# Performance work log

Hardware: AMD Instinct MI355X
Metric: run time of the kernel (lower is better)

## Reference

```python
import jax, jax.numpy as jnp
import numpy as np

N_NODES = 100000


def gcn_conv(x, src, dst, norm, W, b):
    # PyG GCNConv: linear transform first, then normalized scatter-add aggregation, then bias.
    xw = x @ W                                   # [N, out]
    msgs = xw[src] * norm[:, None]               # [E+N, out] gathered, degree-normalized messages
    out = jax.ops.segment_sum(msgs, dst, num_segments=N_NODES)
    return out + b


def _build_graph(edge_index):
    # add self-loops (PyG gcn_norm default)
    loop = jnp.arange(N_NODES, dtype=edge_index.dtype)
    src = jnp.concatenate([edge_index[0], loop])
    dst = jnp.concatenate([edge_index[1], loop])
    deg = jax.ops.segment_sum(jnp.ones_like(dst, dtype=jnp.float32), dst, num_segments=N_NODES)
    dis = jnp.where(deg > 0, jax.lax.rsqrt(jnp.maximum(deg, 1.0)), 0.0)
    norm = dis[src] * dis[dst]                   # D^-1/2 (A+I) D^-1/2 edge weights
    return src, dst, norm


def setup_inputs() -> dict:
    key = jax.random.key(0)
    ks = jax.random.split(key, 6)
    F_IN, H, C, E = 128, 128, 8, 1600000
    x = jax.random.normal(ks[0], (N_NODES, F_IN), dtype=jnp.float32)
    edge_index = jax.random.randint(ks[1], (2, E), 0, N_NODES, dtype=jnp.int64)
    # glorot-style init for conv weights
    W1 = jax.random.normal(ks[2], (F_IN, H), dtype=jnp.float32) * (1.0 / np.sqrt(F_IN))
    b1 = jnp.zeros((H,), dtype=jnp.float32)
    W2 = jax.random.normal(ks[3], (H, C), dtype=jnp.float32) * (1.0 / np.sqrt(H))
    b2 = jnp.zeros((C,), dtype=jnp.float32)
    return {"x": x, "edge_index": edge_index, "W1": W1, "b1": b1, "W2": W2, "b2": b2}


def reference(x, edge_index, W1, b1, W2, b2):
    src, dst, norm = _build_graph(edge_index)
    h = gcn_conv(x, src, dst, norm, W1, b1)
    h = jax.nn.relu(h)
    # dropout is identity in eval mode
    out = gcn_conv(h, src, dst, norm, W2, b2)
    return jax.nn.log_softmax(out, axis=1)
```

## Files before the change

### kernel.cpp

```cpp
#include <hip/hip_runtime.h>

#define N_NODES 100000
#define NBKT 782
#define EPB 8192
#define SL_STRIDE 800000

typedef unsigned int uint;

__device__ __forceinline__ uint pack_bf16_2(float a, float b) {
    uint ua = __float_as_uint(a), ub = __float_as_uint(b);
    ua += 0x7fff + ((ua >> 16) & 1);
    ub += 0x7fff + ((ub >> 16) & 1);
    return (ua >> 16) | (ub & 0xffff0000u);
}
__device__ __forceinline__ float bf_lo(uint u) { return __uint_as_float(u << 16); }
__device__ __forceinline__ float bf_hi(uint u) { return __uint_as_float(u & 0xffff0000u); }

__device__ __forceinline__ int edge_at(const int* __restrict__ ei, int idx, int is64) {
    return is64 ? ei[2 * idx] : ei[idx];
}

__global__ void k_zero(int* __restrict__ bkt_cnt, int* __restrict__ flag,
                       const int* __restrict__ ei, float* __restrict__ y2) {
    int i = blockIdx.x * 256 + threadIdx.x;
    if (i < NBKT) bkt_cnt[i] = 0;
    if (i < N_NODES * 8) y2[i] = 0.0f;
    if (blockIdx.x == 0) {
        if (threadIdx.x == 0) flag[0] = 0;
        __syncthreads();
        int any = 0;
        for (int j = threadIdx.x; j < 4096; j += 256) any |= ei[2 * j + 1];
        if (any) atomicOr(flag, 1);
    }
}

__global__ __launch_bounds__(256) void kA1(const int* __restrict__ ei, int E,
                                           const int* __restrict__ flag,
                                           int* __restrict__ bkt_cnt) {
    __shared__ int h[NBKT];
    int t = threadIdx.x;
    for (int i = t; i < NBKT; i += 256) h[i] = 0;
    __syncthreads();
    int is64 = (flag[0] == 0);
    int base = blockIdx.x * EPB;
    int end = min(base + EPB, E);
    for (int e = base + t; e < end; e += 256) {
        int d = edge_at(ei, E + e, is64);
        atomicAdd(&h[d >> 7], 1);
    }
    __syncthreads();
    for (int i = t; i < NBKT; i += 256)
        if (h[i]) atomicAdd(&bkt_cnt[i], h[i]);
}

__global__ __launch_bounds__(1024) void kA2(const int* __restrict__ bkt_cnt,
                                            int* __restrict__ bkt_off,
                                            int* __restrict__ bkt_cursor) {
    __shared__ int s[1024];
    int t = threadIdx.x;
    int v = (t < NBKT) ? bkt_cnt[t] : 0;
    s[t] = v;
    __syncthreads();
    for (int d = 1; d < 1024; d <<= 1) {
        int y = (t >= d) ? s[t - d] : 0;
        __syncthreads();
        s[t] += y;
        __syncthreads();
    }
    if (t < NBKT) {
        int o = s[t] - v;
        bkt_off[t] = o;
        bkt_cursor[t] = o;
    }
}

__global__ __launch_bounds__(256) void kA3(const int* __restrict__ ei, int E,
                                           const int* __restrict__ flag,
                                           int* __restrict__ bkt_cursor,
                                           uint* __restrict__ bkt_data) {
    __shared__ int h[NBKT];
    __shared__ int base[NBKT];
    int t = threadIdx.x;
    for (int i = t; i < NBKT; i += 256) h[i] = 0;
    __syncthreads();
    int is64 = (flag[0] == 0);
    int lo = blockIdx.x * EPB;
    int end = min(lo + EPB, E);
    for (int e = lo + t; e < end; e += 256) {
        int d = edge_at(ei, E + e, is64);
        atomicAdd(&h[d >> 7], 1);
    }
    __syncthreads();
    for (int i = t; i < NBKT; i += 256) {
        int c = h[i];
        base[i] = c ? atomicAdd(&bkt_cursor[i], c) : 0;
    }
    __syncthreads();
    for (int i = t; i < NBKT; i += 256) h[i] = 0;
    __syncthreads();
    for (int e = lo + t; e < end; e += 256) {
        int d = edge_at(ei, E + e, is64);
        int s = edge_at(ei, e, is64);
        int b = d >> 7;
        int r = atomicAdd(&h[b], 1);
        bkt_data[base[b] + r] = ((uint)s << 7) | (uint)(d & 127);
    }
}

__global__ __launch_bounds__(256) void kB(const uint* __restrict__ bkt_data,
                                          const int* __restrict__ bkt_off,
                                          const int* __restrict__ bkt_cnt,
                                          int* __restrict__ srcs,
                                          int* __restrict__ count,
                                          int* __restrict__ offs,
                                          float* __restrict__ dis) {
    __shared__ int lc[128];
    __shared__ int sc[128];
    __shared__ int lcur[128];
    int t = threadIdx.x;
    int b = blockIdx.x;
    if (t < 128) { lc[t] = 0; lcur[t] = 0; }
    __syncthreads();
    int start = bkt_off[b];
    int n = bkt_cnt[b];
    for (int i = t; i < n; i += 256)
        atomicAdd(&lc[bkt_data[start + i] & 127], 1);
    __syncthreads();
    if (t < 128) sc[t] = lc[t];
    __syncthreads();
    for (int d = 1; d < 128; d <<= 1) {
        int y = 0;
        if (t < 128 && t >= d) y = sc[t - d];
        __syncthreads();
        if (t < 128) sc[t] += y;
        __syncthreads();
    }
    if (t < 128) {
        int node = b * 128 + t;
        if (node < N_NODES) {
            int c = lc[t];
            count[node] = c;
            offs[node] = start + sc[t] - c;
            dis[node] = rsqrtf((float)c + 1.0f);
        }
    }
    __syncthreads();
    for (int i = t; i < n; i += 256) {
        uint rec = bkt_data[start + i];
        int dl = rec & 127;
        int r = atomicAdd(&lcur[dl], 1);
        srcs[start + (sc[dl] - lc[dl]) + r] = rec >> 7;
    }
}

__global__ __launch_bounds__(256) void k_gemm1(const float* __restrict__ x,
                                               const float* __restrict__ W,
                                               const float* __restrict__ dis,
                                               uint* __restrict__ y1s) {
    __shared__ float Wl[64 * 128];
    __shared__ float Xl[32 * 128];
    int t = threadIdx.x;
    int row0 = blockIdx.x * 32;

    const float4* X4 = (const float4*)(x + (size_t)row0 * 128);
    float4* Xl4 = (float4*)Xl;
#pragma unroll
    for (int i = 0; i < 4; ++i) Xl4[t + 256 * i] = X4[t + 256 * i];

    int cg = t & 31;
    int rg = t >> 5;
    float acc[4][4] = {};
    float4* Wl4 = (float4*)Wl;
    const float4* W4 = (const float4*)W;

    for (int kh = 0; kh < 2; ++kh) {
        __syncthreads();
#pragma unroll
        for (int i = 0; i < 8; ++i) Wl4[t + 256 * i] = W4[kh * 2048 + t + 256 * i];
        __syncthreads();
        for (int k = 0; k < 64; ++k) {
            float4 w = Wl4[k * 32 + cg];
#pragma unroll
            for (int r = 0; r < 4; ++r) {
                float xv = Xl[(4 * rg + r) * 128 + kh * 64 + k];
                acc[r][0] = fmaf(xv, w.x, acc[r][0]);
                acc[r][1] = fmaf(xv, w.y, acc[r][1]);
                acc[r][2] = fmaf(xv, w.z, acc[r][2]);
                acc[r][3] = fmaf(xv, w.w, acc[r][3]);
            }
        }
    }
    int slice = cg >> 2, sp = cg & 3;
#pragma unroll
    for (int r = 0; r < 4; ++r) {
        int row = row0 + 4 * rg + r;
        float dd = dis[row];
        uint2 o;
        o.x = pack_bf16_2(acc[r][0] * dd, acc[r][1] * dd);
        o.y = pack_bf16_2(acc[r][2] * dd, acc[r][3] * dd);
        ((uint2*)y1s)[(size_t)slice * (SL_STRIDE / 2) + row * 4 + sp] = o;
    }
}

__global__ __launch_bounds__(256) void k_agg1s(const uint* __restrict__ y1s,
                                               const int* __restrict__ srcs,
                                               const int* __restrict__ offs,
                                               const int* __restrict__ count,
                                               const float* __restrict__ dis,
                                               const float* __restrict__ b1,
                                               const float* __restrict__ W2,
                                               float* __restrict__ y2) {
    int t = threadIdx.x;
    int slice = blockIdx.x & 7;
    int nb = blockIdx.x >> 3;
    int g = t >> 3;
    int j = t & 7;
    int d = nb * 32 + g;

    float w0[8], w1[8];
    const float* wr0 = W2 + (size_t)(slice * 16 + 2 * j) * 8;
#pragma unroll
    for (int c = 0; c < 8; ++c) { w0[c] = wr0[c]; w1[c] = wr0[8 + c]; }

    const uint4* ybase = (const uint4*)(y1s + (size_t)slice * SL_STRIDE);
    float acc[16];
#pragma unroll
    for (int c = 0; c < 16; ++c) acc[c] = 0.0f;

    int st = offs[d], n = count[d];
    for (int i = j; i <= n; i += 8) {
        int sk = d;
        if (i < n) sk = srcs[st + i];
        uint4 a  = ybase[(size_t)sk * 2];
        uint4 bq = ybase[(size_t)sk * 2 + 1];
        acc[0]  += bf_lo(a.x);  acc[1]  += bf_hi(a.x);
        acc[2]  += bf_lo(a.y);  acc[3]  += bf_hi(a.y);
        acc[4]  += bf_lo(a.z);  acc[5]  += bf_hi(a.z);
        acc[6]  += bf_lo(a.w);  acc[7]  += bf_hi(a.w);
        acc[8]  += bf_lo(bq.x); acc[9]  += bf_hi(bq.x);
        acc[10] += bf_lo(bq.y); acc[11] += bf_hi(bq.y);
        acc[12] += bf_lo(bq.z); acc[13] += bf_hi(bq.z);
        acc[14] += bf_lo(bq.w); acc[15] += bf_hi(bq.w);
    }

    int hi4 = (j >> 2) & 1, hi2 = (j >> 1) & 1, hi1 = j & 1;
    float v8[8];
#pragma unroll
    for (int c = 0; c < 8; ++c) {
        float keep = hi4 ? acc[c + 8] : acc[c];
        float send = hi4 ? acc[c] : acc[c + 8];
        v8[c] = keep + __shfl_xor(send, 4, 8);
    }
    float v4[4];
#pragma unroll
    for (int c = 0; c < 4; ++c) {
        float keep = hi2 ? v8[c + 4] : v8[c];
        float send = hi2 ? v8[c] : v8[c + 4];
        v4[c] = keep + __shfl_xor(send, 2, 8);
    }
    float v2[2];
#pragma unroll
    for (int c = 0; c < 2; ++c) {
        float keep = hi1 ? v4[c + 2] : v4[c];
        float send = hi1 ? v4[c] : v4[c + 2];
        v2[c] = keep + __shfl_xor(send, 1, 8);
    }

    float dd = dis[d];
    float2 b = ((const float2*)b1)[slice * 8 + j];
    float h0 = fmaxf(fmaf(v2[0], dd, b.x), 0.0f);
    float h1 = fmaxf(fmaf(v2[1], dd, b.y), 0.0f);

    float p[8];
#pragma unroll
    for (int c = 0; c < 8; ++c) p[c] = h0 * w0[c] + h1 * w1[c];
    float q4[4];
#pragma unroll
    for (int c = 0; c < 4; ++c) {
        float keep = hi4 ? p[c + 4] : p[c];
        float send = hi4 ? p[c] : p[c + 4];
        q4[c] = keep + __shfl_xor(send, 4, 8);
    }
    float q2[2];
#pragma unroll
    for (int c = 0; c < 2; ++c) {
        float keep = hi2 ? q4[c + 2] : q4[c];
        float send = hi2 ? q4[c] : q4[c + 2];
        q2[c] = keep + __shfl_xor(send, 2, 8);
    }
    float keep = hi1 ? q2[1] : q2[0];
    float send = hi1 ? q2[0] : q2[1];
    float q = keep + __shfl_xor(send, 1, 8);

    atomicAdd(&y2[(size_t)d * 8 + j], q * dd);
}

__global__ __launch_bounds__(256) void k_agg2(const float* __restrict__ y2,
                                              const int* __restrict__ srcs,
                                              const int* __restrict__ offs,
                                              const int* __restrict__ count,
                                              const float* __restrict__ dis,
                                              const float* __restrict__ b2,
                                              float* __restrict__ out) {
    int g = (blockIdx.x * 256 + threadIdx.x) >> 3;
    int c = threadIdx.x & 7;
    if (g >= N_NODES) return;
    float acc = y2[(size_t)g * 8 + c];
    float acc2 = 0.0f;
    int st = offs[g], n = count[g];
    int i = 0;
    for (; i + 2 <= n; i += 2) {
        int s0 = srcs[st + i], s1 = srcs[st + i + 1];
        acc  += y2[(size_t)s0 * 8 + c];
        acc2 += y2[(size_t)s1 * 8 + c];
    }
    if (i < n) acc += y2[(size_t)srcs[st + i] * 8 + c];
    acc += acc2;

    float o = fmaf(acc, dis[g], b2[c]);
    float m = o;
#pragma unroll
    for (int k = 1; k < 8; k <<= 1) m = fmaxf(m, __shfl_xor(m, k, 64));
    float e = expf(o - m);
    float ssum = e;
#pragma unroll
    for (int k = 1; k < 8; k <<= 1) ssum += __shfl_xor(ssum, k, 64);
    out[(size_t)g * 8 + c] = (o - m) - logf(ssum);
}

extern "C" void kernel_launch(void* const* d_in, const int* in_sizes, int n_in,
                              void* d_out, int out_size, void* d_ws, size_t ws_size,
                              hipStream_t stream) {
    const float* x  = (const float*)d_in[0];
    const int*   ei = (const int*)d_in[1];
    const float* W1 = (const float*)d_in[2];
    const float* b1 = (const float*)d_in[3];
    const float* W2 = (const float*)d_in[4];
    const float* b2 = (const float*)d_in[5];
    float* out = (float*)d_out;
    const int E = in_sizes[1] / 2;

    char* ws = (char*)d_ws;
    int*   flag       = (int*)ws;
    int*   bkt_cnt    = (int*)(ws + 256);
    int*   bkt_off    = bkt_cnt + 784;
    int*   bkt_cursor = bkt_off + 784;
    int*   count      = bkt_cursor + 784;
    int*   offs       = count + N_NODES;
    float* dis        = (float*)(offs + N_NODES);
    uint*  bkt_data   = (uint*)(dis + N_NODES);
    int*   srcs       = (int*)(bkt_data + E);
    uint*  y1s        = (uint*)(srcs + E);
    float* y2         = (float*)(y1s + (size_t)8 * SL_STRIDE);

    const int PB = (E + EPB - 1) / EPB;

    k_zero <<<3125, 256, 0, stream>>>(bkt_cnt, flag, ei, y2);
    kA1    <<<PB, 256, 0, stream>>>(ei, E, flag, bkt_cnt);
    kA2    <<<1, 1024, 0, stream>>>(bkt_cnt, bkt_off, bkt_cursor);
    kA3    <<<PB, 256, 0, stream>>>(ei, E, flag, bkt_cursor, bkt_data);
    kB     <<<NBKT, 256, 0, stream>>>(bkt_data, bkt_off, bkt_cnt, srcs, count, offs, dis);

    k_gemm1<<<N_NODES / 32, 256, 0, stream>>>(x, W1, dis, y1s);
    k_agg1s<<<8 * 3125, 256, 0, stream>>>(y1s, srcs, offs, count, dis, b1, W2, y2);
    k_agg2 <<<(N_NODES + 31) / 32, 256, 0, stream>>>(y2, srcs, offs, count, dis, b2, out);
}
```

Baseline: 226.1 us.

## Use bf16 MFMA for first GEMM, unroll aggregation gather, vectorize zeroing

```diff
diff --git a/kernel.cpp b/kernel.cpp
--- a/kernel.cpp
+++ b/kernel.cpp
@@ -6,6 +6,10 @@
 #define SL_STRIDE 800000
 
 typedef unsigned int uint;
+typedef __attribute__((ext_vector_type(8))) short bf16x8;
+typedef __attribute__((ext_vector_type(4))) float f32x4;
+
+union FragU { uint4 u; bf16x8 b; };
 
 __device__ __forceinline__ uint pack_bf16_2(float a, float b) {
     uint ua = __float_as_uint(a), ub = __float_as_uint(b);
@@ -21,10 +25,10 @@
 }
 
 __global__ void k_zero(int* __restrict__ bkt_cnt, int* __restrict__ flag,
-                       const int* __restrict__ ei, float* __restrict__ y2) {
+                       const int* __restrict__ ei, float4* __restrict__ y2q) {
     int i = blockIdx.x * 256 + threadIdx.x;
     if (i < NBKT) bkt_cnt[i] = 0;
-    if (i < N_NODES * 8) y2[i] = 0.0f;
+    if (i < N_NODES * 2) y2q[i] = make_float4(0.f, 0.f, 0.f, 0.f);
     if (blockIdx.x == 0) {
         if (threadIdx.x == 0) flag[0] = 0;
         __syncthreads();
@@ -157,48 +161,80 @@
                                                const float* __restrict__ W,
                                                const float* __restrict__ dis,
                                                uint* __restrict__ y1s) {
-    __shared__ float Wl[64 * 128];
-    __shared__ float Xl[32 * 128];
-    int t = threadIdx.x;
-    int row0 = blockIdx.x * 32;
-
-    const float4* X4 = (const float4*)(x + (size_t)row0 * 128);
-    float4* Xl4 = (float4*)Xl;
-#pragma unroll
-    for (int i = 0; i < 4; ++i) Xl4[t + 256 * i] = X4[t + 256 * i];
-
-    int cg = t & 31;
-    int rg = t >> 5;
-    float acc[4][4] = {};
-    float4* Wl4 = (float4*)Wl;
+    __shared__ uint4 WtA[2048];
+    char* wt = (char*)WtA;
+    int t = threadIdx.x;
+
     const float4* W4 = (const float4*)W;
-
-    for (int kh = 0; kh < 2; ++kh) {
-        __syncthreads();
-#pragma unroll
-        for (int i = 0; i < 8; ++i) Wl4[t + 256 * i] = W4[kh * 2048 + t + 256 * i];
-        __syncthreads();
-        for (int k = 0; k < 64; ++k) {
-            float4 w = Wl4[k * 32 + cg];
-#pragma unroll
-            for (int r = 0; r < 4; ++r) {
-                float xv = Xl[(4 * rg + r) * 128 + kh * 64 + k];
-                acc[r][0] = fmaf(xv, w.x, acc[r][0]);
-                acc[r][1] = fmaf(xv, w.y, acc[r][1]);
-                acc[r][2] = fmaf(xv, w.z, acc[r][2]);
-                acc[r][3] = fmaf(xv, w.w, acc[r][3]);
+#pragma unroll
+    for (int ii = 0; ii < 4; ++ii) {
+        int tile = t + 256 * ii;
+        int nq = tile >> 5, kq = tile & 31;
+        float4 r0 = W4[(4 * kq + 0) * 32 + nq];
+        float4 r1 = W4[(4 * kq + 1) * 32 + nq];
+        float4 r2 = W4[(4 * kq + 2) * 32 + nq];
+        float4 r3 = W4[(4 * kq + 3) * 32 + nq];
+        const float* p0 = (const float*)&r0;
+        const float* p1 = (const float*)&r1;
+        const float* p2 = (const float*)&r2;
+        const float* p3 = (const float*)&r3;
+#pragma unroll
+        for (int cc = 0; cc < 4; ++cc) {
+            int n = 4 * nq + cc;
+            uint2 v;
+            v.x = pack_bf16_2(p0[cc], p1[cc]);
+            v.y = pack_bf16_2(p2[cc], p3[cc]);
+            *(uint2*)(wt + n * 256 + (((kq >> 1) ^ (n & 7)) << 4) + ((kq & 1) << 3)) = v;
+        }
+    }
+    __syncthreads();
+
+    int w = t >> 6, lane = t & 63;
+    int m = lane & 15, kg = lane >> 4;
+    int row0 = blockIdx.x * 64 + 16 * w;
+
+    int arow = row0 + m;
+    bool av = arow < N_NODES;
+    const float4* xr = (const float4*)(x + (size_t)arow * 128);
+    float4 z4 = make_float4(0.f, 0.f, 0.f, 0.f);
+    FragU af[4];
+#pragma unroll
+    for (int kf = 0; kf < 4; ++kf) {
+        float4 g0 = av ? xr[8 * kf + 2 * kg]     : z4;
+        float4 g1 = av ? xr[8 * kf + 2 * kg + 1] : z4;
+        const float* a0 = (const float*)&g0;
+        const float* a1 = (const float*)&g1;
+        af[kf].u.x = pack_bf16_2(a0[0], a0[1]);
+        af[kf].u.y = pack_bf16_2(a0[2], a0[3]);
+        af[kf].u.z = pack_bf16_2(a1[0], a1[1]);
+        af[kf].u.w = pack_bf16_2(a1[2], a1[3]);
+    }
+
+    int crow = row0 + 4 * kg;
+    float dd[4];
+#pragma unroll
+    for (int rr = 0; rr < 4; ++rr)
+        dd[rr] = (crow + rr < N_NODES) ? dis[crow + rr] : 0.0f;
+
+#pragma unroll
+    for (int ct = 0; ct < 8; ++ct) {
+        f32x4 acc = {0.f, 0.f, 0.f, 0.f};
+#pragma unroll
+        for (int kf = 0; kf < 4; ++kf) {
+            int n = 16 * ct + m;
+            bf16x8 bw = *(const bf16x8*)(wt + n * 256 + ((((kf << 2) | kg) ^ (n & 7)) << 4));
+            acc = __builtin_amdgcn_mfma_f32_16x16x32_bf16(af[kf].b, bw, acc, 0, 0, 0);
+        }
+#pragma unroll
+        for (int rr = 0; rr < 4; ++rr) {
+            float v = acc[rr] * dd[rr];
+            float p = __shfl_xor(v, 1, 64);
+            if (!(lane & 1)) {
+                int grow = crow + rr;
+                if (grow < N_NODES)
+                    y1s[(size_t)ct * SL_STRIDE + grow * 8 + (m >> 1)] = pack_bf16_2(v, p);
             }
         }
-    }
-    int slice = cg >> 2, sp = cg & 3;
-#pragma unroll
-    for (int r = 0; r < 4; ++r) {
-        int row = row0 + 4 * rg + r;
-        float dd = dis[row];
-        uint2 o;
-        o.x = pack_bf16_2(acc[r][0] * dd, acc[r][1] * dd);
-        o.y = pack_bf16_2(acc[r][2] * dd, acc[r][3] * dd);
-        ((uint2*)y1s)[(size_t)slice * (SL_STRIDE / 2) + row * 4 + sp] = o;
     }
 }
 
@@ -228,10 +264,26 @@
     for (int c = 0; c < 16; ++c) acc[c] = 0.0f;
 
     int st = offs[d], n = count[d];
-    for (int i = j; i <= n; i += 8) {
-        int sk = d;
-        if (i < n) sk = srcs[st + i];
-        uint4 a  = ybase[(size_t)sk * 2];
+    int i = j;
+    for (; i + 8 <= n; i += 16) {
+        int s0 = srcs[st + i];
+        int s1 = (i + 8 < n) ? srcs[st + i + 8] : d;
+        uint4 a0 = ybase[(size_t)s0 * 2];
+        uint4 b0 = ybase[(size_t)s0 * 2 + 1];
+        uint4 a1 = ybase[(size_t)s1 * 2];
+        uint4 b1q = ybase[(size_t)s1 * 2 + 1];
+        acc[0]  += bf_lo(a0.x) + bf_lo(a1.x);  acc[1]  += bf_hi(a0.x) + bf_hi(a1.x);
+        acc[2]  += bf_lo(a0.y) + bf_lo(a1.y);  acc[3]  += bf_hi(a0.y) + bf_hi(a1.y);
+        acc[4]  += bf_lo(a0.z) + bf_lo(a1.z);  acc[5]  += bf_hi(a0.z) + bf_hi(a1.z);
+        acc[6]  += bf_lo(a0.w) + bf_lo(a1.w);  acc[7]  += bf_hi(a0.w) + bf_hi(a1.w);
+        acc[8]  += bf_lo(b0.x) + bf_lo(b1q.x); acc[9]  += bf_hi(b0.x) + bf_hi(b1q.x);
+        acc[10] += bf_lo(b0.y) + bf_lo(b1q.y); acc[11] += bf_hi(b0.y) + bf_hi(b1q.y);
+        acc[12] += bf_lo(b0.z) + bf_lo(b1q.z); acc[13] += bf_hi(b0.z) + bf_hi(b1q.z);
+        acc[14] += bf_lo(b0.w) + bf_lo(b1q.w); acc[15] += bf_hi(b0.w) + bf_hi(b1q.w);
+    }
+    if (i <= n) {
+        int sk = (i < n) ? srcs[st + i] : d;
+        uint4 a = ybase[(size_t)sk * 2];
         uint4 bq = ybase[(size_t)sk * 2 + 1];
         acc[0]  += bf_lo(a.x);  acc[1]  += bf_hi(a.x);
         acc[2]  += bf_lo(a.y);  acc[3]  += bf_hi(a.y);
@@ -266,10 +318,10 @@
         v2[c] = keep + __shfl_xor(send, 1, 8);
     }
 
-    float dd = dis[d];
+    float ddv = dis[d];
     float2 b = ((const float2*)b1)[slice * 8 + j];
-    float h0 = fmaxf(fmaf(v2[0], dd, b.x), 0.0f);
-    float h1 = fmaxf(fmaf(v2[1], dd, b.y), 0.0f);
+    float h0 = fmaxf(fmaf(v2[0], ddv, b.x), 0.0f);
+    float h1 = fmaxf(fmaf(v2[1], ddv, b.y), 0.0f);
 
     float p[8];
 #pragma unroll
@@ -292,7 +344,7 @@
     float send = hi1 ? q2[0] : q2[1];
     float q = keep + __shfl_xor(send, 1, 8);
 
-    atomicAdd(&y2[(size_t)d * 8 + j], q * dd);
+    atomicAdd(&y2[(size_t)d * 8 + j], q * ddv);
 }
 
 __global__ __launch_bounds__(256) void k_agg2(const float* __restrict__ y2,
@@ -355,13 +407,13 @@
 
     const int PB = (E + EPB - 1) / EPB;
 
-    k_zero <<<3125, 256, 0, stream>>>(bkt_cnt, flag, ei, y2);
+    k_zero <<<782, 256, 0, stream>>>(bkt_cnt, flag, ei, (float4*)y2);
     kA1    <<<PB, 256, 0, stream>>>(ei, E, flag, bkt_cnt);
     kA2    <<<1, 1024, 0, stream>>>(bkt_cnt, bkt_off, bkt_cursor);
     kA3    <<<PB, 256, 0, stream>>>(ei, E, flag, bkt_cursor, bkt_data);
     kB     <<<NBKT, 256, 0, stream>>>(bkt_data, bkt_off, bkt_cnt, srcs, count, offs, dis);
 
-    k_gemm1<<<N_NODES / 32, 256, 0, stream>>>(x, W1, dis, y1s);
+    k_gemm1<<<(N_NODES + 63) / 64, 256, 0, stream>>>(x, W1, dis, y1s);
     k_agg1s<<<8 * 3125, 256, 0, stream>>>(y1s, srcs, offs, count, dis, b1, W2, y2);
     k_agg2 <<<(N_NODES + 31) / 32, 256, 0, stream>>>(y2, srcs, offs, count, dis, b2, out);
 }
```

Result: no change. 227.1 us (+0.5%).
